# Kernel tuning notes

Hardware: AMD Instinct MI355X
Metric: run time of the kernel (lower is better)

The kernel has to match this reference:

```python
import jax, jax.numpy as jnp
import numpy as np

N = 100_000      # nodes
E = 3_200_000    # edges (avg degree 32)
D = 128          # input_dim == hidden_dim
L = 3            # num_layers
G = 64           # number of graphs in the batch
EPS = 1e-5       # LayerNorm eps


def setup_inputs() -> dict:
    key = jax.random.key(0)
    ks = jax.random.split(key, 8)
    x = jax.random.normal(ks[0], (N, D), dtype=jnp.float32)
    edge_index = jax.random.randint(ks[1], (2, E), 0, N, dtype=jnp.int64)
    edge_weight = jax.random.normal(ks[2], (E,), dtype=jnp.float32)
    batch = jnp.sort(jax.random.randint(ks[3], (N,), 0, G, dtype=jnp.int64))
    s = 1.0 / np.sqrt(D)
    W_pos = jax.random.normal(ks[4], (L, D, D), dtype=jnp.float32) * s
    W_neg = jax.random.normal(ks[5], (L, D, D), dtype=jnp.float32) * s
    b_pos = jnp.zeros((L, D), dtype=jnp.float32)
    b_neg = jnp.zeros((L, D), dtype=jnp.float32)
    gamma = jnp.ones((D,), dtype=jnp.float32)
    beta = jnp.zeros((D,), dtype=jnp.float32)
    return dict(x=x, edge_index=edge_index, edge_weight=edge_weight, batch=batch,
                W_pos=W_pos, b_pos=b_pos, W_neg=W_neg, b_neg=b_neg,
                gamma=gamma, beta=beta)


def _branch_norm(src, dst, mask, n):
    # GCN symmetric normalization on the masked subgraph with unit edge weights
    # and self-loops (fill_value=1). deg counted on target nodes (PyG col).
    deg = 1.0 + jax.ops.segment_sum(mask, dst, num_segments=n)  # >= 1
    dinv_sqrt = jax.lax.rsqrt(deg)
    edge_norm = mask * dinv_sqrt[src] * dinv_sqrt[dst]          # 0 on masked-out edges
    self_norm = 1.0 / deg                                       # self-loop coefficient
    return edge_norm, self_norm


def _gcn_layer(h, W, b, src, dst, edge_norm, self_norm):
    h = h @ W  # [N, H], lin without bias (PyG GCNConv)
    agg = jax.ops.segment_sum(edge_norm[:, None] * h[src], dst,
                              num_segments=h.shape[0])
    return agg + h * self_norm[:, None] + b


def reference(x, edge_index, edge_weight, batch, W_pos, b_pos, W_neg, b_neg, gamma, beta):
    src, dst = edge_index[0], edge_index[1]
    pos_mask = (edge_weight > 0).astype(x.dtype)
    neg_mask = (edge_weight < 0).astype(x.dtype)
    n = x.shape[0]
    pos_en, pos_sn = _branch_norm(src, dst, pos_mask, n)
    neg_en, neg_sn = _branch_norm(src, dst, neg_mask, n)
    h = x
    for l in range(W_pos.shape[0]):
        hp = _gcn_layer(h, W_pos[l], b_pos[l], src, dst, pos_en, pos_sn)
        hn = _gcn_layer(h, W_neg[l], b_neg[l], src, dst, neg_en, neg_sn)
        h = jax.nn.relu(hp) - jax.nn.relu(hn)
    # global mean pool over graphs
    counts = jax.ops.segment_sum(jnp.ones((n,), h.dtype), batch, num_segments=G)
    sums = jax.ops.segment_sum(h, batch, num_segments=G)
    pooled = sums / jnp.clip(counts, 1.0)[:, None]  # [G, H]
    # LayerNorm
    mu = jnp.mean(pooled, axis=-1, keepdims=True)
    var = jnp.mean(jnp.square(pooled - mu), axis=-1, keepdims=True)
    return (pooled - mu) * jax.lax.rsqrt(var + EPS) * gamma + beta
```

## Files before the change

### kernel.cpp

```cpp
#include <hip/hip_runtime.h>
#include <stdint.h>

typedef unsigned short u16;
typedef __attribute__((ext_vector_type(8))) short bfrag;
typedef __attribute__((ext_vector_type(4))) float f32x4;
typedef __attribute__((ext_vector_type(2))) float f32x2;

__device__ __forceinline__ uint32_t pack2bf(float x, float y) {
  uint32_t bx = __float_as_uint(x), by = __float_as_uint(y);
  bx += 0x7fffu + ((bx >> 16) & 1u);
  by += 0x7fffu + ((by >> 16) & 1u);
  return (bx >> 16) | (by & 0xffff0000u);
}
__device__ __forceinline__ u16 f2bf(float x) {
  uint32_t b = __float_as_uint(x);
  b += 0x7fffu + ((b >> 16) & 1u);
  return (u16)(b >> 16);
}
__device__ __forceinline__ float bflo(uint32_t p) { return __uint_as_float(p << 16); }
__device__ __forceinline__ float bfhi(uint32_t p) { return __uint_as_float(p & 0xffff0000u); }

__global__ void k_cvt_x(const float* __restrict__ x, uint32_t* __restrict__ xb,
                        uint32_t* __restrict__ x8, int n4) {
  int i = blockIdx.x * blockDim.x + threadIdx.x;
  if (i >= n4) return;
  float4 v = ((const float4*)x)[i];
  xb[2 * i]     = pack2bf(v.x, v.y);
  xb[2 * i + 1] = pack2bf(v.z, v.w);
  uint32_t p8 = __builtin_amdgcn_cvt_pk_fp8_f32(v.x, v.y, 0u, false);
  p8 = __builtin_amdgcn_cvt_pk_fp8_f32(v.z, v.w, p8, true);
  x8[i] = p8;
}

__global__ void k_cvt_w(const float* __restrict__ wp, const float* __restrict__ wn,
                        u16* __restrict__ wt, int total) {
  int i = blockIdx.x * blockDim.x + threadIdx.x;
  if (i >= total) return;
  int l = i >> 15;
  int rem = i & 32767;
  int br = rem >> 14;
  int rem2 = rem & 16383;
  int c = rem2 >> 7;
  int k = rem2 & 127;
  const float* w = br ? wn : wp;
  wt[i] = f2bf(w[l * 16384 + k * 128 + c]);
}

__global__ __launch_bounds__(256) void k_histA(
    const int* __restrict__ ei, const float* __restrict__ ew,
    int* __restrict__ histA, int E, int nbk, int nba) {
  __shared__ int h[1600];
  int blk = blockIdx.x, t = threadIdx.x;
  for (int b = t; b < nbk; b += 256) h[b] = 0;
  __syncthreads();
  int base = blk * 8192;
  int lim = base + 8192; if (lim > E) lim = E;
  for (int e = base + t; e < lim; e += 256) {
    if (ew[e] == 0.f) continue;
    atomicAdd(&h[ei[E + e] >> 6], 1);
  }
  __syncthreads();
  for (int b = t; b < nbk; b += 256) histA[(size_t)b * nba + blk] = h[b];
}

__global__ void k_scan1(const int* __restrict__ cnt, int* __restrict__ offs,
                        int* __restrict__ part, int M) {
  __shared__ int sh[1024];
  int t = threadIdx.x;
  int i = blockIdx.x * 1024 + t;
  int v = (i < M) ? cnt[i] : 0;
  sh[t] = v;
  __syncthreads();
  for (int off = 1; off < 1024; off <<= 1) {
    int add = (t >= off) ? sh[t - off] : 0;
    __syncthreads();
    sh[t] += add;
    __syncthreads();
  }
  if (i < M) offs[i] = sh[t] - v;
  if (t == 1023) part[blockIdx.x] = sh[1023];
}
__global__ void k_scan2(int* __restrict__ part, int* __restrict__ offs,
                        uint32_t* __restrict__ recF, int nb, int M) {
  __shared__ int sh[1024];
  int t = threadIdx.x;
  int v = (t < nb) ? part[t] : 0;
  sh[t] = v;
  __syncthreads();
  for (int off = 1; off < 1024; off <<= 1) {
    int add = (t >= off) ? sh[t - off] : 0;
    __syncthreads();
    sh[t] += add;
    __syncthreads();
  }
  if (t < nb) part[t] = sh[t] - v;
  if (t == 1023) {
    int run = sh[1023];
    offs[M] = run;
    for (int i = 0; i < 32; ++i) recF[run + i] = 0u;
  }
}

__global__ __launch_bounds__(256) void k_partB(
    const int* __restrict__ ei, const float* __restrict__ ew,
    const int* __restrict__ offsA, const int* __restrict__ partA,
    uint32_t* __restrict__ rec4, int E, int nbk, int nba) {
  __shared__ int curs[1600];
  int blk = blockIdx.x, t = threadIdx.x;
  for (int b = t; b < nbk; b += 256) {
    int idx = b * nba + blk;
    curs[b] = offsA[idx] + partA[idx >> 10];
  }
  __syncthreads();
  int base = blk * 8192;
  int lim = base + 8192; if (lim > E) lim = E;
  for (int e = base + t; e < lim; e += 256) {
    float w = ew[e];
    if (w == 0.f) continue;
    int s = ei[e], d = ei[E + e];
    int pos = atomicAdd(&curs[d >> 6], 1);
    rec4[pos] = (uint32_t)s | ((w < 0.f ? 1u : 0u) << 17) | ((uint32_t)(d & 63) << 18);
  }
}

__global__ __launch_bounds__(256) void k_sortC(
    const uint32_t* __restrict__ rec4, const int* __restrict__ offsA,
    const int* __restrict__ partA, uint32_t* __restrict__ recF,
    int* __restrict__ bnd2, float* __restrict__ dpn,
    int n, int nbk, int nba, int SM) {
  __shared__ uint32_t rin[3072];
  __shared__ uint32_t rout[3072];
  __shared__ int hist[128];
  __shared__ int curs[128];
  int b = blockIdx.x, t = threadIdx.x;
  int i0 = b * nba;
  int beg = offsA[i0] + partA[i0 >> 10];
  int end;
  if (b + 1 < nbk) {
    int i1 = (b + 1) * nba;
    end = offsA[i1] + partA[i1 >> 10];
  } else {
    end = offsA[SM];
  }
  int cnt = end - beg;
  if (cnt > 3072) cnt = 3072;
  for (int i = t; i < cnt; i += 256) rin[i] = rec4[beg + i];
  if (t < 128) hist[t] = 0;
  __syncthreads();
  for (int i = t; i < cnt; i += 256)
    atomicAdd(&hist[(rin[i] >> 17) & 127], 1);
  __syncthreads();
  if (t == 0) {
    int run = 0;
    for (int k = 0; k < 128; ++k) { int c = hist[k]; curs[k] = run; run += c; }
  }
  __syncthreads();
  if (t < 64) {
    int node = b * 64 + t;
    if (node < n) {
      bnd2[2 * node]     = beg + curs[t * 2];
      bnd2[2 * node + 1] = beg + curs[t * 2 + 1];
      int degp = hist[t * 2], degn = hist[t * 2 + 1];
      dpn[2 * node]     = rsqrtf(1.f + (float)degp);
      dpn[2 * node + 1] = rsqrtf(1.f + (float)degn);
    }
  }
  if (t == 0 && b == nbk - 1) bnd2[2 * n] = end;
  __syncthreads();
  for (int i = t; i < cnt; i += 256) {
    uint32_t r = rin[i];
    int pos = atomicAdd(&curs[(r >> 17) & 127], 1);
    rout[pos] = r & 0x1FFFFu;
  }
  __syncthreads();
  for (int i = t; i < cnt; i += 256) recF[beg + i] = rout[i];
}

__global__ __launch_bounds__(256) void k_agg(
    const uint32_t* __restrict__ hin, const uint8_t* __restrict__ x8,
    const int* __restrict__ bnd2,
    const uint32_t* __restrict__ rec, const float* __restrict__ dpn,
    uint32_t* __restrict__ up, uint32_t* __restrict__ un, int n) {
  int gid = blockIdx.x * blockDim.x + threadIdx.x;
  int nd = gid >> 6, lane = gid & 63;
  if (nd >= n) return;
  int beg = bnd2[2 * nd], mid = bnd2[2 * nd + 1], end = bnd2[2 * nd + 2];
  float ap0 = 0.f, ap1 = 0.f, an0 = 0.f, an1 = 0.f;
  for (int j = beg; j < mid; j += 8) {
    uint32_t rr[8]; float dd[8]; u16 pk[8];
#pragma unroll
    for (int u = 0; u < 8; ++u) rr[u] = rec[j + u];
#pragma unroll
    for (int u = 0; u < 8; ++u) dd[u] = dpn[rr[u] * 2];
#pragma unroll
    for (int u = 0; u < 8; ++u)
      pk[u] = *(const u16*)(x8 + (size_t)rr[u] * 128 + lane * 2);
#pragma unroll
    for (int u = 0; u < 8; ++u) {
      float nm = (j + u < mid) ? dd[u] : 0.f;
      f32x2 v = __builtin_amdgcn_cvt_pk_f32_fp8((uint32_t)pk[u], false);
      ap0 = fmaf(nm, v.x, ap0);
      ap1 = fmaf(nm, v.y, ap1);
    }
  }
  for (int j = mid; j < end; j += 8) {
    uint32_t rr[8]; float dd[8]; u16 pk[8];
#pragma unroll
    for (int u = 0; u < 8; ++u) rr[u] = rec[j + u];
#pragma unroll
    for (int u = 0; u < 8; ++u) dd[u] = dpn[rr[u] * 2 + 1];
#pragma unroll
    for (int u = 0; u < 8; ++u)
      pk[u] = *(const u16*)(x8 + (size_t)rr[u] * 128 + lane * 2);
#pragma unroll
    for (int u = 0; u < 8; ++u) {
      float nm = (j + u < end) ? dd[u] : 0.f;
      f32x2 v = __builtin_amdgcn_cvt_pk_f32_fp8((uint32_t)pk[u], false);
      an0 = fmaf(nm, v.x, an0);
      an1 = fmaf(nm, v.y, an1);
    }
  }
  float dpd = dpn[2 * nd], dnd = dpn[2 * nd + 1];
  float sp = dpd * dpd, sn = dnd * dnd;
  uint32_t hk = hin[(size_t)nd * 64 + lane];
  float h0 = bflo(hk), h1 = bfhi(hk);
  up[(size_t)nd * 64 + lane] = pack2bf(fmaf(sp, h0, dpd * ap0), fmaf(sp, h1, dpd * ap1));
  un[(size_t)nd * 64 + lane] = pack2bf(fmaf(sn, h0, dnd * an0), fmaf(sn, h1, dnd * an1));
}

__global__ __launch_bounds__(256, 2) void k_gemm(
    const short* __restrict__ up, const short* __restrict__ un,
    const u16* __restrict__ wt, const float* __restrict__ bp, const float* __restrict__ bn,
    u16* __restrict__ hout, uint8_t* __restrict__ x8out, int nrows, int nchunks) {
  __shared__ __align__(16) u16 wl[32768];
  __shared__ __align__(16) u16 ct[4][8][132];
  __shared__ __align__(16) uint8_t ct8[4][8][144];
  int t = threadIdx.x;
  for (int i = t; i < 4096; i += 256) {
    int ci = i & 2047;
    int col = ci >> 4, kc16 = ci & 15;
    int db = (i >> 11) * 32768 + ((col * 256 + kc16 * 16) ^ ((col & 7) << 4));
    *(uint4*)((char*)wl + db) = ((const uint4*)wt)[i];
  }
  __syncthreads();
  int wv = t >> 6, lane = t & 63;
  int l15 = lane & 15, l4 = lane >> 4;
  float vbp[8], vbn[8];
#pragma unroll
  for (int nt = 0; nt < 8; ++nt) {
    vbp[nt] = bp[nt * 16 + l15];
    vbn[nt] = bn[nt * 16 + l15];
  }
  for (int c = blockIdx.x; c < nchunks; c += gridDim.x) {
    int rowbase = c * 128 + wv * 32;
    int r0 = rowbase + l15;      if (r0 >= nrows) r0 = nrows - 1;
    int r1 = rowbase + 16 + l15; if (r1 >= nrows) r1 = nrows - 1;
    f32x4 accP[2][8], accN[2][8];
#pragma unroll
    for (int rt = 0; rt < 2; ++rt)
#pragma unroll
      for (int nt = 0; nt < 8; ++nt) { accP[rt][nt] = (f32x4)(0.f); accN[rt][nt] = (f32x4)(0.f); }
#pragma unroll
    for (int kc = 0; kc < 4; ++kc) {
      int koff = kc * 32 + l4 * 8;
      bfrag aP0 = *(const bfrag*)(up + (size_t)r0 * 128 + koff);
      bfrag aP1 = *(const bfrag*)(up + (size_t)r1 * 128 + koff);
      bfrag aN0 = *(const bfrag*)(un + (size_t)r0 * 128 + koff);
      bfrag aN1 = *(const bfrag*)(un + (size_t)r1 * 128 + koff);
#pragma unroll
      for (int nt = 0; nt < 8; ++nt) {
        int col = nt * 16 + l15;
        int bb = (col * 256 + kc * 64 + l4 * 16) ^ ((col & 7) << 4);
        bfrag bP = *(const bfrag*)((const char*)wl + bb);
        bfrag bN = *(const bfrag*)((const char*)wl + 32768 + bb);
        accP[0][nt] = __builtin_amdgcn_mfma_f32_16x16x32_bf16(aP0, bP, accP[0][nt], 0, 0, 0);
        accP[1][nt] = __builtin_amdgcn_mfma_f32_16x16x32_bf16(aP1, bP, accP[1][nt], 0, 0, 0);
        accN[0][nt] = __builtin_amdgcn_mfma_f32_16x16x32_bf16(aN0, bN, accN[0][nt], 0, 0, 0);
        accN[1][nt] = __builtin_amdgcn_mfma_f32_16x16x32_bf16(aN1, bN, accN[1][nt], 0, 0, 0);
      }
    }
#pragma unroll
    for (int rt = 0; rt < 2; ++rt) {
#pragma unroll
      for (int h = 0; h < 2; ++h) {
        if ((l4 >> 1) == h) {
          int lr = (l4 & 1) * 4;
#pragma unroll
          for (int nt = 0; nt < 8; ++nt) {
            int col = nt * 16 + l15;
#pragma unroll
            for (int r = 0; r < 4; ++r) {
              float vp = accP[rt][nt][r] + vbp[nt]; vp = vp > 0.f ? vp : 0.f;
              float vn = accN[rt][nt][r] + vbn[nt]; vn = vn > 0.f ? vn : 0.f;
              float hv = vp - vn;
              ct[wv][lr + r][col] = f2bf(hv);
              ct8[wv][lr + r][col] =
                  (uint8_t)(__builtin_amdgcn_cvt_pk_fp8_f32(hv, hv, 0u, false) & 0xffu);
            }
          }
        }
#pragma unroll
        for (int i = 0; i < 2; ++i) {
          int lrow = i * 4 + (l4 & 3);
          int grow = rowbase + rt * 16 + h * 8 + lrow;
          uint4 vv = *(const uint4*)&ct[wv][lrow][l15 * 8];
          if (grow < nrows)
            *(uint4*)(hout + (size_t)grow * 128 + l15 * 8) = vv;
        }
        {
          int lrow = lane >> 3, lch = lane & 7;
          int grow = rowbase + rt * 16 + h * 8 + lrow;
          uint4 b16 = *(const uint4*)&ct8[wv][lrow][lch * 16];
          if (grow < nrows)
            *(uint4*)(x8out + (size_t)grow * 128 + lch * 16) = b16;
        }
      }
    }
  }
}

__global__ void k_pool(const uint32_t* __restrict__ h, const int* __restrict__ batch,
                       float* __restrict__ pooled, float* __restrict__ gcnt, int n) {
  int gid = blockIdx.x * blockDim.x + threadIdx.x;
  int w = gid >> 6, lane = gid & 63;
  int n0 = w * 8;
  if (n0 >= n) return;
  int curg = -1, c = 0;
  float a0 = 0.f, a1 = 0.f;
  for (int i = 0; i < 8; ++i) {
    int nd = n0 + i;
    if (nd >= n) break;
    int g = batch[nd];
    if (g != curg) {
      if (curg >= 0) {
        atomicAdd(&pooled[curg * 128 + 2 * lane], a0);
        atomicAdd(&pooled[curg * 128 + 2 * lane + 1], a1);
        if (lane == 0) atomicAdd(gcnt + curg, (float)c);
      }
      curg = g; a0 = a1 = 0.f; c = 0;
    }
    uint32_t pk = h[(size_t)nd * 64 + lane];
    a0 += bflo(pk); a1 += bfhi(pk); ++c;
  }
  if (curg >= 0) {
    atomicAdd(&pooled[curg * 128 + 2 * lane], a0);
    atomicAdd(&pooled[curg * 128 + 2 * lane + 1], a1);
    if (lane == 0) atomicAdd(gcnt + curg, (float)c);
  }
}

__global__ void k_ln(const float* __restrict__ pooled, const float* __restrict__ gcnt,
                     const float* __restrict__ gamma, const float* __restrict__ beta,
                     float* __restrict__ out, int G) {
  int gid = blockIdx.x * blockDim.x + threadIdx.x;
  int g = gid >> 6, lane = gid & 63;
  if (g >= G) return;
  float2 s = ((const float2*)pooled)[g * 64 + lane];
  float cm = fmaxf(gcnt[g], 1.f);
  float v0 = s.x / cm, v1 = s.y / cm;
  float tsum = v0 + v1;
#pragma unroll
  for (int m = 1; m < 64; m <<= 1) tsum += __shfl_xor(tsum, m, 64);
  float mu = tsum * (1.f / 128.f);
  float d0 = v0 - mu, d1 = v1 - mu;
  float q = d0 * d0 + d1 * d1;
#pragma unroll
  for (int m = 1; m < 64; m <<= 1) q += __shfl_xor(q, m, 64);
  float inv = rsqrtf(q * (1.f / 128.f) + 1e-5f);
  int f = 2 * lane;
  out[g * 128 + f]     = d0 * inv * gamma[f]     + beta[f];
  out[g * 128 + f + 1] = d1 * inv * gamma[f + 1] + beta[f + 1];
}

extern "C" void kernel_launch(void* const* d_in, const int* in_sizes, int n_in,
                              void* d_out, int out_size, void* d_ws, size_t ws_size,
                              hipStream_t stream) {
  const float* x     = (const float*)d_in[0];
  const int* ei      = (const int*)d_in[1];
  const float* ew    = (const float*)d_in[2];
  const int* bt      = (const int*)d_in[3];
  const float* Wp    = (const float*)d_in[4];
  const float* bp    = (const float*)d_in[5];
  const float* Wn    = (const float*)d_in[6];
  const float* bn    = (const float*)d_in[7];
  const float* gamma = (const float*)d_in[8];
  const float* beta  = (const float*)d_in[9];
  int N = in_sizes[0] / 128;
  int E = in_sizes[1] / 2;
  int L = in_sizes[4] / (128 * 128);
  int G = out_size / 128;
  int nbk = (N + 63) / 64;
  int nba = (E + 8191) / 8192;
  int SM = nbk * nba;

  char* w = (char*)d_ws;
  auto alloc = [&](size_t bytes) {
    char* p = w;
    w += (bytes + 255) & ~(size_t)255;
    return p;
  };
  uint32_t* X    = (uint32_t*)alloc((size_t)N * 128 * 2);
  uint8_t* X8    = (uint8_t*)alloc((size_t)N * 128 + 256);
  uint32_t* U    = (uint32_t*)alloc((size_t)N * 128 * 2);
  uint32_t* V    = (uint32_t*)alloc((size_t)N * 128 * 2);
  u16* wt        = (u16*)alloc((size_t)L * 2 * 128 * 128 * 2);
  uint32_t* rec4 = (uint32_t*)alloc(((size_t)E + 32) * 4);
  uint32_t* recF = (uint32_t*)alloc(((size_t)E + 32) * 4);
  int* histA     = (int*)alloc((size_t)SM * 4);
  int* offsA     = (int*)alloc((size_t)(SM + 1) * 4);
  int* partA     = (int*)alloc(1024 * 4);
  int* bnd2      = (int*)alloc((size_t)(2 * N + 1) * 4);
  float* dpn     = (float*)alloc((size_t)N * 8);
  float* pooled  = (float*)alloc((size_t)G * 128 * 4);
  float* gcnt    = (float*)alloc((size_t)G * 4);

  hipMemsetAsync(pooled, 0, (size_t)G * 128 * 4, stream);
  hipMemsetAsync(gcnt, 0, (size_t)G * 4, stream);

  int n4 = N * 32;
  int wtot = L * 2 * 128 * 128;
  k_cvt_x<<<(n4 + 255) / 256, 256, 0, stream>>>(x, X, (uint32_t*)X8, n4);
  k_cvt_w<<<(wtot + 255) / 256, 256, 0, stream>>>(Wp, Wn, wt, wtot);
  k_histA<<<nba, 256, 0, stream>>>(ei, ew, histA, E, nbk, nba);
  int NB1 = (SM + 1023) / 1024;
  k_scan1<<<NB1, 1024, 0, stream>>>(histA, offsA, partA, SM);
  k_scan2<<<1, 1024, 0, stream>>>(partA, offsA, recF, NB1, SM);
  k_partB<<<nba, 256, 0, stream>>>(ei, ew, offsA, partA, rec4, E, nbk, nba);
  k_sortC<<<nbk, 256, 0, stream>>>(rec4, offsA, partA, recF, bnd2, dpn, N, nbk, nba, SM);

  int nchunks = (N + 127) / 128;
  for (int l = 0; l < L; ++l) {
    k_agg<<<((size_t)N * 64 + 255) / 256, 256, 0, stream>>>(X, X8, bnd2, recF, dpn, U, V, N);
    k_gemm<<<512, 256, 0, stream>>>((const short*)U, (const short*)V,
                                    wt + (size_t)l * 32768, bp + (size_t)l * 128,
                                    bn + (size_t)l * 128, (u16*)X, X8, N, nchunks);
  }
  k_pool<<<(((N + 7) / 8) * 64 + 255) / 256, 256, 0, stream>>>(X, bt, pooled, gcnt, N);
  k_ln<<<(G * 64 + 255) / 256, 256, 0, stream>>>(pooled, gcnt, gamma, beta, (float*)d_out, G);
}
```

Before: 595.8 us.

## Prescale fp8 gather tables by source degree norms per branch

Builds two fp8 shadow copies of node features, one already multiplied by each node's positive-branch rsqrt degree and one by its negative-branch rsqrt degree. The aggregation then only sums gathered rows and no longer does a dependent per-edge dpn load and multiply. The GEMM epilogue writes both scaled fp8 tables, which doubles fp8 write traffic and epilogue work and adds an extra shadow kernel. Scaling before fp8 quantization also changes the rounding behaviour.

```diff
diff --git a/kernel.cpp b/kernel.cpp
--- a/kernel.cpp
+++ b/kernel.cpp
@@ -20,16 +20,26 @@
 __device__ __forceinline__ float bflo(uint32_t p) { return __uint_as_float(p << 16); }
 __device__ __forceinline__ float bfhi(uint32_t p) { return __uint_as_float(p & 0xffff0000u); }
 
-__global__ void k_cvt_x(const float* __restrict__ x, uint32_t* __restrict__ xb,
-                        uint32_t* __restrict__ x8, int n4) {
+__global__ void k_cvt_x(const float* __restrict__ x, uint32_t* __restrict__ xb, int n4) {
   int i = blockIdx.x * blockDim.x + threadIdx.x;
   if (i >= n4) return;
   float4 v = ((const float4*)x)[i];
   xb[2 * i]     = pack2bf(v.x, v.y);
   xb[2 * i + 1] = pack2bf(v.z, v.w);
-  uint32_t p8 = __builtin_amdgcn_cvt_pk_fp8_f32(v.x, v.y, 0u, false);
-  p8 = __builtin_amdgcn_cvt_pk_fp8_f32(v.z, v.w, p8, true);
-  x8[i] = p8;
+}
+
+__global__ void k_shadow(const uint32_t* __restrict__ xb, const float* __restrict__ dpn,
+                         uint8_t* __restrict__ x8p, uint8_t* __restrict__ x8n, int n) {
+  int gid = blockIdx.x * blockDim.x + threadIdx.x;
+  int nd = gid >> 6, lane = gid & 63;
+  if (nd >= n) return;
+  float dp = dpn[2 * nd], dn = dpn[2 * nd + 1];
+  uint32_t pk = xb[(size_t)nd * 64 + lane];
+  float v0 = bflo(pk), v1 = bfhi(pk);
+  *(u16*)(x8p + (size_t)nd * 128 + lane * 2) =
+      (u16)(__builtin_amdgcn_cvt_pk_fp8_f32(dp * v0, dp * v1, 0u, false) & 0xffffu);
+  *(u16*)(x8n + (size_t)nd * 128 + lane * 2) =
+      (u16)(__builtin_amdgcn_cvt_pk_fp8_f32(dn * v0, dn * v1, 0u, false) & 0xffffu);
 }
 
 __global__ void k_cvt_w(const float* __restrict__ wp, const float* __restrict__ wn,
@@ -177,9 +187,10 @@
 }
 
 __global__ __launch_bounds__(256) void k_agg(
-    const uint32_t* __restrict__ hin, const uint8_t* __restrict__ x8,
-    const int* __restrict__ bnd2,
-    const uint32_t* __restrict__ rec, const float* __restrict__ dpn,
+    const uint32_t* __restrict__ hin,
+    const uint8_t* __restrict__ x8p, const uint8_t* __restrict__ x8n,
+    const int* __restrict__ bnd2, const uint32_t* __restrict__ rec,
+    const float* __restrict__ dpn,
     uint32_t* __restrict__ up, uint32_t* __restrict__ un, int n) {
   int gid = blockIdx.x * blockDim.x + threadIdx.x;
   int nd = gid >> 6, lane = gid & 63;
@@ -187,37 +198,33 @@
   int beg = bnd2[2 * nd], mid = bnd2[2 * nd + 1], end = bnd2[2 * nd + 2];
   float ap0 = 0.f, ap1 = 0.f, an0 = 0.f, an1 = 0.f;
   for (int j = beg; j < mid; j += 8) {
-    uint32_t rr[8]; float dd[8]; u16 pk[8];
+    uint32_t rr[8]; u16 pk[8];
 #pragma unroll
     for (int u = 0; u < 8; ++u) rr[u] = rec[j + u];
 #pragma unroll
-    for (int u = 0; u < 8; ++u) dd[u] = dpn[rr[u] * 2];
-#pragma unroll
     for (int u = 0; u < 8; ++u)
-      pk[u] = *(const u16*)(x8 + (size_t)rr[u] * 128 + lane * 2);
+      pk[u] = *(const u16*)(x8p + (size_t)rr[u] * 128 + lane * 2);
 #pragma unroll
     for (int u = 0; u < 8; ++u) {
-      float nm = (j + u < mid) ? dd[u] : 0.f;
-      f32x2 v = __builtin_amdgcn_cvt_pk_f32_fp8((uint32_t)pk[u], false);
-      ap0 = fmaf(nm, v.x, ap0);
-      ap1 = fmaf(nm, v.y, ap1);
+      u16 pm = (j + u < mid) ? pk[u] : (u16)0;
+      f32x2 v = __builtin_amdgcn_cvt_pk_f32_fp8((uint32_t)pm, false);
+      ap0 += v.x;
+      ap1 += v.y;
     }
   }
   for (int j = mid; j < end; j += 8) {
-    uint32_t rr[8]; float dd[8]; u16 pk[8];
+    uint32_t rr[8]; u16 pk[8];
 #pragma unroll
     for (int u = 0; u < 8; ++u) rr[u] = rec[j + u];
 #pragma unroll
-    for (int u = 0; u < 8; ++u) dd[u] = dpn[rr[u] * 2 + 1];
-#pragma unroll
     for (int u = 0; u < 8; ++u)
-      pk[u] = *(const u16*)(x8 + (size_t)rr[u] * 128 + lane * 2);
+      pk[u] = *(const u16*)(x8n + (size_t)rr[u] * 128 + lane * 2);
 #pragma unroll
     for (int u = 0; u < 8; ++u) {
-      float nm = (j + u < end) ? dd[u] : 0.f;
-      f32x2 v = __builtin_amdgcn_cvt_pk_f32_fp8((uint32_t)pk[u], false);
-      an0 = fmaf(nm, v.x, an0);
-      an1 = fmaf(nm, v.y, an1);
+      u16 pm = (j + u < end) ? pk[u] : (u16)0;
+      f32x2 v = __builtin_amdgcn_cvt_pk_f32_fp8((uint32_t)pm, false);
+      an0 += v.x;
+      an1 += v.y;
     }
   }
   float dpd = dpn[2 * nd], dnd = dpn[2 * nd + 1];
@@ -231,7 +238,9 @@
 __global__ __launch_bounds__(256, 2) void k_gemm(
     const short* __restrict__ up, const short* __restrict__ un,
     const u16* __restrict__ wt, const float* __restrict__ bp, const float* __restrict__ bn,
-    u16* __restrict__ hout, uint8_t* __restrict__ x8out, int nrows, int nchunks) {
+    const float* __restrict__ dpn,
+    u16* __restrict__ hout, uint8_t* __restrict__ x8p, uint8_t* __restrict__ x8n,
+    int nrows, int nchunks) {
   __shared__ __align__(16) u16 wl[32768];
   __shared__ __align__(16) u16 ct[4][8][132];
   __shared__ __align__(16) uint8_t ct8[4][8][144];
@@ -286,16 +295,19 @@
         if ((l4 >> 1) == h) {
           int lr = (l4 & 1) * 4;
 #pragma unroll
-          for (int nt = 0; nt < 8; ++nt) {
-            int col = nt * 16 + l15;
-#pragma unroll
-            for (int r = 0; r < 4; ++r) {
+          for (int r = 0; r < 4; ++r) {
+            int rw = rowbase + rt * 16 + h * 8 + lr + r;
+            if (rw >= nrows) rw = nrows - 1;
+            float dpr = dpn[2 * rw];
+#pragma unroll
+            for (int nt = 0; nt < 8; ++nt) {
+              int col = nt * 16 + l15;
               float vp = accP[rt][nt][r] + vbp[nt]; vp = vp > 0.f ? vp : 0.f;
               float vn = accN[rt][nt][r] + vbn[nt]; vn = vn > 0.f ? vn : 0.f;
               float hv = vp - vn;
               ct[wv][lr + r][col] = f2bf(hv);
               ct8[wv][lr + r][col] =
-                  (uint8_t)(__builtin_amdgcn_cvt_pk_fp8_f32(hv, hv, 0u, false) & 0xffu);
+                  (uint8_t)(__builtin_amdgcn_cvt_pk_fp8_f32(dpr * hv, dpr * hv, 0u, false) & 0xffu);
             }
           }
         }
@@ -312,7 +324,32 @@
           int grow = rowbase + rt * 16 + h * 8 + lrow;
           uint4 b16 = *(const uint4*)&ct8[wv][lrow][lch * 16];
           if (grow < nrows)
-            *(uint4*)(x8out + (size_t)grow * 128 + lch * 16) = b16;
+            *(uint4*)(x8p + (size_t)grow * 128 + lch * 16) = b16;
+        }
+        if ((l4 >> 1) == h) {
+          int lr = (l4 & 1) * 4;
+#pragma unroll
+          for (int r = 0; r < 4; ++r) {
+            int rw = rowbase + rt * 16 + h * 8 + lr + r;
+            if (rw >= nrows) rw = nrows - 1;
+            float dnr = dpn[2 * rw + 1];
+#pragma unroll
+            for (int nt = 0; nt < 8; ++nt) {
+              int col = nt * 16 + l15;
+              float vp = accP[rt][nt][r] + vbp[nt]; vp = vp > 0.f ? vp : 0.f;
+              float vn = accN[rt][nt][r] + vbn[nt]; vn = vn > 0.f ? vn : 0.f;
+              float hv = vp - vn;
+              ct8[wv][lr + r][col] =
+                  (uint8_t)(__builtin_amdgcn_cvt_pk_fp8_f32(dnr * hv, dnr * hv, 0u, false) & 0xffu);
+            }
+          }
+        }
+        {
+          int lrow = lane >> 3, lch = lane & 7;
+          int grow = rowbase + rt * 16 + h * 8 + lrow;
+          uint4 b16 = *(const uint4*)&ct8[wv][lrow][lch * 16];
+          if (grow < nrows)
+            *(uint4*)(x8n + (size_t)grow * 128 + lch * 16) = b16;
         }
       }
     }
@@ -400,7 +437,8 @@
     return p;
   };
   uint32_t* X    = (uint32_t*)alloc((size_t)N * 128 * 2);
-  uint8_t* X8    = (uint8_t*)alloc((size_t)N * 128 + 256);
+  uint8_t* X8p   = (uint8_t*)alloc((size_t)N * 128 + 256);
+  uint8_t* X8n   = (uint8_t*)alloc((size_t)N * 128 + 256);
   uint32_t* U    = (uint32_t*)alloc((size_t)N * 128 * 2);
   uint32_t* V    = (uint32_t*)alloc((size_t)N * 128 * 2);
   u16* wt        = (u16*)alloc((size_t)L * 2 * 128 * 128 * 2);
@@ -419,7 +457,7 @@
 
   int n4 = N * 32;
   int wtot = L * 2 * 128 * 128;
-  k_cvt_x<<<(n4 + 255) / 256, 256, 0, stream>>>(x, X, (uint32_t*)X8, n4);
+  k_cvt_x<<<(n4 + 255) / 256, 256, 0, stream>>>(x, X, n4);
   k_cvt_w<<<(wtot + 255) / 256, 256, 0, stream>>>(Wp, Wn, wt, wtot);
   k_histA<<<nba, 256, 0, stream>>>(ei, ew, histA, E, nbk, nba);
   int NB1 = (SM + 1023) / 1024;
@@ -427,13 +465,14 @@
   k_scan2<<<1, 1024, 0, stream>>>(partA, offsA, recF, NB1, SM);
   k_partB<<<nba, 256, 0, stream>>>(ei, ew, offsA, partA, rec4, E, nbk, nba);
   k_sortC<<<nbk, 256, 0, stream>>>(rec4, offsA, partA, recF, bnd2, dpn, N, nbk, nba, SM);
+  k_shadow<<<((size_t)N * 64 + 255) / 256, 256, 0, stream>>>(X, dpn, X8p, X8n, N);
 
   int nchunks = (N + 127) / 128;
   for (int l = 0; l < L; ++l) {
-    k_agg<<<((size_t)N * 64 + 255) / 256, 256, 0, stream>>>(X, X8, bnd2, recF, dpn, U, V, N);
+    k_agg<<<((size_t)N * 64 + 255) / 256, 256, 0, stream>>>(X, X8p, X8n, bnd2, recF, dpn, U, V, N);
     k_gemm<<<512, 256, 0, stream>>>((const short*)U, (const short*)V,
                                     wt + (size_t)l * 32768, bp + (size_t)l * 128,
-                                    bn + (size_t)l * 128, (u16*)X, X8, N, nchunks);
+                                    bn + (size_t)l * 128, dpn, (u16*)X, X8p, X8n, N, nchunks);
   }
   k_pool<<<(((N + 7) / 8) * 64 + 255) / 256, 256, 0, stream>>>(X, bt, pooled, gcnt, N);
   k_ln<<<(G * 64 + 255) / 256, 256, 0, stream>>>(pooled, gcnt, gamma, beta, (float*)d_out, G);
```

New measurement: 632.2 us. 6.1% more time.
